# Kernel optimization log

Hardware: AMD Instinct MI355X
Metric: run time of the kernel (lower is better)

Reference implementation:

```python
import jax, jax.numpy as jnp
import numpy as np

T, B, I, H = 2048, 512, 10, 20  # seq_len, batch, input_size, hidden_size
G = 4 * H  # gate dim, PyTorch order: i, f, g, o


def _lstm_scan(x, w_ih, w_hh, b_ih, b_hh):
    # x: [T, B, I]; w_ih: [4H, I]; w_hh: [4H, H]; biases: [4H]
    # Precompute input projection for all timesteps (one big GEMM).
    x_proj = jnp.einsum('tbi,gi->tbg', x, w_ih) + b_ih + b_hh  # [T, B, 4H]

    def step(carry, xg):
        h, c = carry
        gates = xg + h @ w_hh.T  # [B, 4H]
        i, f, g, o = jnp.split(gates, 4, axis=-1)
        i = jax.nn.sigmoid(i)
        f = jax.nn.sigmoid(f)
        g = jnp.tanh(g)
        o = jax.nn.sigmoid(o)
        c = f * c + i * g
        h = o * jnp.tanh(c)
        return (h, c), h

    h0 = jnp.zeros((x.shape[1], H), x.dtype)
    c0 = jnp.zeros((x.shape[1], H), x.dtype)
    _, hs = jax.lax.scan(step, (h0, c0), x_proj)
    return hs  # [T, B, H]


def setup_inputs() -> dict:
    key = jax.random.key(0)
    ks = jax.random.split(key, 9)
    s_ih = 1.0 / np.sqrt(H)
    inp = {
        'x': jax.random.normal(ks[0], (T, B, I, 1), dtype=jnp.float32),
        'w_ih_f': jax.random.uniform(ks[1], (G, I), jnp.float32, -s_ih, s_ih),
        'w_hh_f': jax.random.uniform(ks[2], (G, H), jnp.float32, -s_ih, s_ih),
        'b_ih_f': jax.random.uniform(ks[3], (G,), jnp.float32, -s_ih, s_ih),
        'b_hh_f': jax.random.uniform(ks[4], (G,), jnp.float32, -s_ih, s_ih),
        'w_ih_r': jax.random.uniform(ks[5], (G, I), jnp.float32, -s_ih, s_ih),
        'w_hh_r': jax.random.uniform(ks[6], (G, H), jnp.float32, -s_ih, s_ih),
        'b_ih_r': jax.random.uniform(ks[7], (G,), jnp.float32, -s_ih, s_ih),
        'b_hh_r': jax.random.uniform(ks[8], (G,), jnp.float32, -s_ih, s_ih),
    }
    return inp


def reference(x, w_ih_f, w_hh_f, b_ih_f, b_hh_f, w_ih_r, w_hh_r, b_ih_r, b_hh_r):
    xs = jnp.squeeze(x, -1)  # [T, B, I]
    out_f = _lstm_scan(xs, w_ih_f, w_hh_f, b_ih_f, b_hh_f)            # forward dir
    out_r = _lstm_scan(xs[::-1], w_ih_r, w_hh_r, b_ih_r, b_hh_r)[::-1]  # reverse dir
    return jnp.concatenate([out_f, out_r], axis=-1)  # [T, B, 2H]
```

## Files before the change

kernel.cpp:

```cpp
#include <hip/hip_runtime.h>

typedef float f2 __attribute__((ext_vector_type(2)));
typedef float f4 __attribute__((ext_vector_type(4)));

#define TT 2048
#define BB 512
#define II 10
#define HH 20
#define CH 32
#define RS 64
#define NCHUNK (TT / CH)

#define LOG2E 1.44269504088896340736f

__device__ __forceinline__ float fexp2(float x) {
#if __has_builtin(__builtin_amdgcn_exp2f)
    return __builtin_amdgcn_exp2f(x);
#else
    return exp2f(x);
#endif
}

__global__ __launch_bounds__(128, 1) void lstm_bidir(
    const float* __restrict__ x,
    const float* __restrict__ w_ih_f, const float* __restrict__ w_hh_f,
    const float* __restrict__ b_ih_f, const float* __restrict__ b_hh_f,
    const float* __restrict__ w_ih_r, const float* __restrict__ w_hh_r,
    const float* __restrict__ b_ih_r, const float* __restrict__ b_hh_r,
    float* __restrict__ out)
{
    const int tid  = threadIdx.x;
    const int wid  = tid >> 6;
    const int lane = tid & 63;
    const int s    = blockIdx.x;

    const int  dirh  = lane >> 5;
    const int  hl    = lane & 31;
    const bool valid = (hl < HH);
    const int  j     = valid ? hl : (HH - 1);

    const float* __restrict__ w_ih = dirh ? w_ih_r : w_ih_f;
    const float* __restrict__ w_hh = dirh ? w_hh_r : w_hh_f;
    const float* __restrict__ b_ih = dirh ? b_ih_r : b_ih_f;
    const float* __restrict__ b_hh = dirh ? b_hh_r : b_hh_f;

    const int t0    = dirh ? (TT - 1) : 0;
    const int xstep = dirh ? -(BB * II) : (BB * II);
    const int ostep = dirh ? -(BB * 2 * HH) : (BB * 2 * HH);
    const int xbase = (t0 * BB + s) * II;

    const float gsc[4] = { -LOG2E, -LOG2E, -2.0f * LOG2E, -LOG2E };

    __shared__ f4    ring[RS][64];
    __shared__ float hstage[CH * 64];

    if (wid == 1) {
        f2 wih[4][5];
        float bs[4];
#pragma unroll
        for (int g = 0; g < 4; ++g) {
            const int r = g * HH + j;
#pragma unroll
            for (int k = 0; k < 5; ++k) {
                f2 w = *(const f2*)(w_ih + r * II + 2 * k);
                wih[g][k] = w * gsc[g];
            }
            bs[g] = (b_ih[r] + b_hh[r]) * gsc[g];
        }

        auto produce8 = [&](int base) {
            f2 xb[8][5];
#pragma unroll
            for (int i = 0; i < 8; ++i) {
                int u = base + i; if (u > TT - 1) u = TT - 1;
                const float* px = x + (xbase + u * xstep);
#pragma unroll
                for (int k = 0; k < 5; ++k) xb[i][k] = *(const f2*)(px + 2 * k);
            }
#pragma unroll
            for (int i = 0; i < 8; ++i) {
                const int u = base + i;
                if (u < TT) {
                    f4 xp;
#pragma unroll
                    for (int g = 0; g < 4; ++g) {
                        f2 p = {bs[g], 0.f};
#pragma unroll
                        for (int k = 0; k < 5; ++k) p += wih[g][k] * xb[i][k];
                        xp[g] = p[0] + p[1];
                    }
                    ring[u & (RS - 1)][lane] = xp;
                }
            }
        };

        produce8(0);  produce8(8);
        produce8(16); produce8(24);
        for (int chunk = 0; chunk < NCHUNK; ++chunk) {
            __syncthreads();
            const int base = (chunk + 1) * CH;
            produce8(base);      produce8(base + 8);
            produce8(base + 16); produce8(base + 24);
        }
    } else {
        __builtin_amdgcn_s_setprio(1);

        f2 whh[4][10];
#pragma unroll
        for (int g = 0; g < 4; ++g) {
            const int r = g * HH + j;
#pragma unroll
            for (int k = 0; k < 10; ++k) {
                f2 w = *(const f2*)(w_hh + r * HH + 2 * k);
                whh[g][k] = w * gsc[g];
            }
        }

        const int obase = (t0 * BB + s) * (2 * HH) + dirh * HH;
        int offd[20], lds_d[20];
#pragma unroll
        for (int q = 0; q < 20; ++q) {
            const int idx = q * 32 + hl;
            const int td  = idx / HH;
            const int jd  = idx - td * HH;
            offd[q]  = obase + td * ostep + jd;
            lds_d[q] = td * 64 + dirh * 32 + jd;
        }

        const int hboff = dirh * 32;

        const float K2 = 2.0f * LOG2E;

        f4 hb[5];
#pragma unroll
        for (int k = 0; k < 5; ++k) hb[k] = f4{0.f, 0.f, 0.f, 0.f};

        float cs = 0.0f;
        int t = 0;

        for (int chunk = 0; chunk < NCHUNK; ++chunk) {
            __syncthreads();
            f4 xp = ring[t & (RS - 1)][lane];
#pragma unroll 4
            for (int i = 0; i < CH; ++i, ++t) {
                f2 a0[4], a1[4];
#pragma unroll
                for (int g = 0; g < 4; ++g) { a0[g] = f2{0.f, 0.f}; a1[g] = f2{0.f, 0.f}; }
#pragma unroll
                for (int k = 0; k < 5; ++k) {
                    const f4 hv = hb[k];
                    f2 lo; lo[0] = hv[0]; lo[1] = hv[1];
                    f2 hi; hi[0] = hv[2]; hi[1] = hv[3];
#pragma unroll
                    for (int g = 0; g < 4; ++g) {
                        a0[g] += whh[g][2 * k]     * lo;
                        a1[g] += whh[g][2 * k + 1] * hi;
                    }
                }
                float u[4];
#pragma unroll
                for (int g = 0; g < 4; ++g) {
                    const f2 a = a0[g] + a1[g];
                    u[g] = (xp[g] + a[0]) + a[1];
                }

                const float ei = fexp2(u[0]);
                const float ef = fexp2(u[1]);
                const float eg = fexp2(u[2]);
                const float eo = fexp2(u[3]);
                const float fg = __builtin_amdgcn_rcpf(1.0f + ef);
                const float r1 = __builtin_amdgcn_rcpf((1.0f + ei) * (1.0f + eg));
                const float km = __builtin_fmaf(K2, eg, -K2) * r1;
                cs = __builtin_fmaf(fg, cs, km);
                const float ec = fexp2(cs);
                const float h  = (1.0f - ec) *
                    __builtin_amdgcn_rcpf((1.0f + eo) * (1.0f + ec));

                xp = ring[(t + 1) & (RS - 1)][lane];

                hstage[i * 64 + lane] = h;
                __builtin_amdgcn_wave_barrier();

#pragma unroll
                for (int k = 0; k < 5; ++k)
                    hb[k] = *(const f4*)&hstage[i * 64 + hboff + 4 * k];
            }

#pragma unroll
            for (int q = 0; q < 20; ++q) {
                const float v = hstage[lds_d[q]];
                out[offd[q]] = v;
                offd[q] += CH * ostep;
            }
        }
    }
}

extern "C" void kernel_launch(void* const* d_in, const int* in_sizes, int n_in,
                              void* d_out, int out_size, void* d_ws, size_t ws_size,
                              hipStream_t stream) {
    const float* xp     = (const float*)d_in[0];
    const float* w_ih_f = (const float*)d_in[1];
    const float* w_hh_f = (const float*)d_in[2];
    const float* b_ih_f = (const float*)d_in[3];
    const float* b_hh_f = (const float*)d_in[4];
    const float* w_ih_r = (const float*)d_in[5];
    const float* w_hh_r = (const float*)d_in[6];
    const float* b_ih_r = (const float*)d_in[7];
    const float* b_hh_r = (const float*)d_in[8];
    float* outp = (float*)d_out;

    hipLaunchKernelGGL(lstm_bidir, dim3(512), dim3(128), 0, stream,
                       xp, w_ih_f, w_hh_f, b_ih_f, b_hh_f,
                       w_ih_r, w_hh_r, b_ih_r, b_hh_r, outp);
}
```

Before: 441.2 us.

## Move output stores to producer wave with double-buffered h staging

Double-buffers the h staging buffer in LDS and hands the global output writes for each finished chunk to the producer wave, which performs them after the next barrier. The recurrent wave's critical path no longer issues global stores. The cost is extra index math in the producer, a final barrier, and a denser staging layout that changes LDS alignment for the f4 reads.

New measurement: 456.7 us. +3.5%, slower.

```diff
diff --git a/kernel.cpp b/kernel.cpp
--- a/kernel.cpp
+++ b/kernel.cpp
@@ -46,13 +46,12 @@
 
     const int t0    = dirh ? (TT - 1) : 0;
     const int xstep = dirh ? -(BB * II) : (BB * II);
-    const int ostep = dirh ? -(BB * 2 * HH) : (BB * 2 * HH);
     const int xbase = (t0 * BB + s) * II;
 
     const float gsc[4] = { -LOG2E, -LOG2E, -2.0f * LOG2E, -LOG2E };
 
     __shared__ f4    ring[RS][64];
-    __shared__ float hstage[CH * 64];
+    __shared__ float hstage[2][CH][2 * HH];
 
     if (wid == 1) {
         f2 wih[4][5];
@@ -94,14 +93,38 @@
             }
         };
 
+        int tdq[20], remq[20], dirq[20], jdq[20];
+#pragma unroll
+        for (int q = 0; q < 20; ++q) {
+            const int idx = q * 64 + lane;
+            tdq[q]  = idx / (2 * HH);
+            remq[q] = idx - tdq[q] * (2 * HH);
+            dirq[q] = remq[q] / HH;
+            jdq[q]  = remq[q] - dirq[q] * HH;
+        }
+
+        auto dump = [&](int c) {
+            const int buf = c & 1;
+#pragma unroll
+            for (int q = 0; q < 20; ++q) {
+                const int tg   = c * CH + tdq[q];
+                const int trow = dirq[q] ? (TT - 1 - tg) : tg;
+                out[(trow * BB + s) * (2 * HH) + dirq[q] * HH + jdq[q]] =
+                    hstage[buf][tdq[q]][remq[q]];
+            }
+        };
+
         produce8(0);  produce8(8);
         produce8(16); produce8(24);
         for (int chunk = 0; chunk < NCHUNK; ++chunk) {
             __syncthreads();
+            if (chunk > 0) dump(chunk - 1);
             const int base = (chunk + 1) * CH;
             produce8(base);      produce8(base + 8);
             produce8(base + 16); produce8(base + 24);
         }
+        __syncthreads();
+        dump(NCHUNK - 1);
     } else {
         __builtin_amdgcn_s_setprio(1);
 
@@ -116,18 +139,8 @@
             }
         }
 
-        const int obase = (t0 * BB + s) * (2 * HH) + dirh * HH;
-        int offd[20], lds_d[20];
-#pragma unroll
-        for (int q = 0; q < 20; ++q) {
-            const int idx = q * 32 + hl;
-            const int td  = idx / HH;
-            const int jd  = idx - td * HH;
-            offd[q]  = obase + td * ostep + jd;
-            lds_d[q] = td * 64 + dirh * 32 + jd;
-        }
-
-        const int hboff = dirh * 32;
+        const int hpos  = dirh * HH + j;
+        const int hboff = dirh * HH;
 
         const float K2 = 2.0f * LOG2E;
 
@@ -140,6 +153,7 @@
 
         for (int chunk = 0; chunk < NCHUNK; ++chunk) {
             __syncthreads();
+            const int buf = chunk & 1;
             f4 xp = ring[t & (RS - 1)][lane];
 #pragma unroll 4
             for (int i = 0; i < CH; ++i, ++t) {
@@ -178,21 +192,15 @@
 
                 xp = ring[(t + 1) & (RS - 1)][lane];
 
-                hstage[i * 64 + lane] = h;
+                if (valid) hstage[buf][i][hpos] = h;
                 __builtin_amdgcn_wave_barrier();
 
 #pragma unroll
                 for (int k = 0; k < 5; ++k)
-                    hb[k] = *(const f4*)&hstage[i * 64 + hboff + 4 * k];
-            }
-
-#pragma unroll
-            for (int q = 0; q < 20; ++q) {
-                const float v = hstage[lds_d[q]];
-                out[offd[q]] = v;
-                offd[q] += CH * ostep;
-            }
-        }
+                    hb[k] = *(const f4*)&hstage[buf][i][hboff + 4 * k];
+            }
+        }
+        __syncthreads();
     }
 }
 
```
